# Optimization experiments

Hardware: AMD Instinct MI355X
Metric: run time of the kernel (lower is better)

Reference implementation:

```python
import jax, jax.numpy as jnp
import numpy as np

B, S, D = 1, 4096, 1024
H, DH = 8, 128
SCALING = 256.0 ** -0.5
SOFTCAP = 50.0
WINDOW = 512
EPS = 1e-6
NEG = -1e30


def setup_inputs() -> dict:
    key = jax.random.key(0)
    ks = jax.random.split(key, 8)
    hidden_states = jax.random.normal(ks[0], (B, S, D), dtype=jnp.float32)
    # rope tables: plausible cos/sin in [-1,1]
    inv_freq = 1.0 / (10000.0 ** (jnp.arange(0, DH, 2, dtype=jnp.float32) / DH))
    t = jnp.arange(S, dtype=jnp.float32)
    freqs = jnp.outer(t, inv_freq)  # [S, DH/2]
    emb = jnp.concatenate([freqs, freqs], axis=-1)  # [S, DH]
    cos = jnp.cos(emb)[None]  # [1, S, DH]
    sin = jnp.sin(emb)[None]
    w = 0.02
    Wq = jax.random.normal(ks[1], (H * DH, D), dtype=jnp.float32) * w
    Wk = jax.random.normal(ks[2], (H * DH, D), dtype=jnp.float32) * w
    Wv = jax.random.normal(ks[3], (H * DH, D), dtype=jnp.float32) * w
    Wo = jax.random.normal(ks[4], (D, H * DH), dtype=jnp.float32) * w
    q_norm_w = jnp.zeros((DH,), dtype=jnp.float32)
    k_norm_w = jnp.zeros((DH,), dtype=jnp.float32)
    return {"hidden_states": hidden_states, "cos": cos, "sin": sin,
            "Wq": Wq, "Wk": Wk, "Wv": Wv, "Wo": Wo,
            "q_norm_w": q_norm_w, "k_norm_w": k_norm_w}


def _rms_norm(x, w):
    # Gemma3 RMSNorm: x * rsqrt(mean(x^2) + eps) * (1 + w)
    var = jnp.mean(jnp.square(x), axis=-1, keepdims=True)
    return x * jax.lax.rsqrt(var + EPS) * (1.0 + w)


def _rotate_half(x):
    x1, x2 = jnp.split(x, 2, axis=-1)
    return jnp.concatenate([-x2, x1], axis=-1)


def reference(hidden_states, cos, sin, Wq, Wk, Wv, Wo, q_norm_w, k_norm_w):
    b, s, _ = hidden_states.shape
    # QKV projections -> [B, H, S, DH]
    q = (hidden_states @ Wq.T).reshape(b, s, H, DH).transpose(0, 2, 1, 3)
    k = (hidden_states @ Wk.T).reshape(b, s, H, DH).transpose(0, 2, 1, 3)
    v = (hidden_states @ Wv.T).reshape(b, s, H, DH).transpose(0, 2, 1, 3)
    # per-head RMSNorm on q and k
    q = _rms_norm(q, q_norm_w)
    k = _rms_norm(k, k_norm_w)
    # RoPE (cos/sin broadcast over heads via unsqueeze(1))
    c = cos[:, None, :, :]
    si = sin[:, None, :, :]
    q = q * c + _rotate_half(q) * si
    k = k * c + _rotate_half(k) * si
    # scores with scaling and logit softcapping
    scores = jnp.einsum('bhqd,bhkd->bhqk', q, k) * SCALING
    scores = SOFTCAP * jnp.tanh(scores / SOFTCAP)
    # causal + sliding-window mask: attend to j with 0 <= i - j < WINDOW (plus j == i)
    i = jnp.arange(s)[:, None]
    j = jnp.arange(s)[None, :]
    mask = (j <= i) & (i - j < WINDOW)  # [S, S]
    scores = jnp.where(mask[None, None], scores, NEG)
    probs = jax.nn.softmax(scores, axis=-1)  # [B, H, S, S]
    attn = jnp.einsum('bhqk,bhkd->bhqd', probs, v)
    attn = attn.transpose(0, 2, 1, 3).reshape(b, s, H * DH)
    out = attn @ Wo.T
    return out, probs
```

## Files before the change

kernel.cpp:

```cpp
#include <hip/hip_runtime.h>

#define S_LEN 4096

typedef _Float16 f16;
typedef __bf16 bf16;
typedef __attribute__((ext_vector_type(4))) _Float16 f16x4;
typedef __attribute__((ext_vector_type(8))) _Float16 f16x8;
typedef __attribute__((ext_vector_type(8))) __bf16 bf16x8;
typedef __attribute__((ext_vector_type(4))) float f32x4;

__device__ __forceinline__ void async_cp16(void* lds, const void* g) {
  __builtin_amdgcn_global_load_lds((const __attribute__((address_space(1))) void*)g,
                                   (__attribute__((address_space(3))) void*)lds, 16, 0, 0);
}

__device__ __forceinline__ f32x4 mfma16(f16x8 a, f16x8 b, f32x4 c) {
  return __builtin_amdgcn_mfma_f32_16x16x32_f16(a, b, c, 0, 0, 0);
}

__global__ void detect_dtype(const unsigned short* __restrict__ x, int* __restrict__ flag) {
  const int t = threadIdx.x;
  int cnt = 0;
  for (int i = t; i < 16384; i += 256) {
    const int e = (x[i] >> 7) & 0xFF;
    cnt += (e >= 0x87);
  }
#pragma unroll
  for (int m = 1; m < 64; m <<= 1) cnt += __shfl_xor(cnt, m);
  __shared__ int red[4];
  if ((t & 63) == 0) red[t >> 6] = cnt;
  __syncthreads();
  if (t == 0) *flag = (red[0] + red[1] + red[2] + red[3] > 64) ? 1 : 0;
}

__device__ __forceinline__ void cvt8(const void* src, f16* dst, int i, int fp) {
  f16x8 o;
  if (fp) {
    const float* s = (const float*)src;
#pragma unroll
    for (int j = 0; j < 8; ++j) o[j] = (f16)s[i + j];
  } else {
    const bf16x8 v = *(const bf16x8*)((const bf16*)src + i);
#pragma unroll
    for (int j = 0; j < 8; ++j) o[j] = (f16)(float)v[j];
  }
  *(f16x8*)(dst + i) = o;
}

__global__ void cvt_all(const void* __restrict__ hs, const void* __restrict__ wq,
                        const void* __restrict__ wk, const void* __restrict__ wv,
                        const void* __restrict__ wo, const void* __restrict__ c,
                        const void* __restrict__ s, const void* __restrict__ qn,
                        const void* __restrict__ kn, f16* __restrict__ hsf,
                        f16* __restrict__ wqkv, f16* __restrict__ woh,
                        float* __restrict__ cd, float* __restrict__ sd,
                        float* __restrict__ qnd, float* __restrict__ knd,
                        const int* __restrict__ flagp) {
  const int fp = *flagp;
  const int b = blockIdx.x, tid = threadIdx.x;
  if (b < 2048) {
    cvt8(hs, hsf, (b * 256 + tid) * 8, fp);
  } else if (b < 4096) {
    const int bb = b - 2048;
    const int sub = bb >> 9;
    const int i = ((bb & 511) * 256 + tid) * 8;
    const void* src = (sub == 0) ? wq : (sub == 1) ? wk : (sub == 2) ? wv : wo;
    f16* dst = (sub < 3) ? (wqkv + (size_t)sub * 1048576) : woh;
    cvt8(src, dst, i, fp);
  } else if (b < 8192) {
    const int bb = b - 4096;
    const void* src = (bb < 2048) ? c : s;
    float* dst = (bb < 2048) ? cd : sd;
    const int i = (bb & 2047) * 256 + tid;
    dst[i] = fp ? ((const float*)src)[i] : (float)((const bf16*)src)[i];
  } else {
    if (tid < 128) qnd[tid] = fp ? ((const float*)qn)[tid] : (float)((const bf16*)qn)[tid];
    else knd[tid - 128] = fp ? ((const float*)kn)[tid - 128] : (float)((const bf16*)kn)[tid - 128];
  }
}

__device__ __forceinline__ void probs_zero_fill(void* dout, int fp, int fb, int nfb) {
  const int tid = threadIdx.x;
  if (fp) {
    float* pb = (float*)dout + 4194304;
    const int total = 8 * 4096 * 880;
    const f32x4 z = {};
    for (int u = fb * 256 + tid; u < total; u += nfb * 256) {
      const int rowid = (int)((unsigned)u / 880u);
      const int cu = u - rowid * 880;
      const int row = rowid & 4095;
      const int q0r = row & ~63;
      const int jc0 = (q0r >= 512) ? (((q0r - 511) >> 6) << 6) : 0;
      const int jc0c = jc0 >> 2;
      const int c4 = (cu < jc0c) ? (cu << 2) : (jc0 + 576 + ((cu - jc0c) << 2));
      __builtin_nontemporal_store(z, (f32x4*)&pb[((size_t)rowid << 12) + c4]);
    }
  } else {
    bf16* pb = (bf16*)dout + 4194304;
    const int total = 8 * 4096 * 440;
    const bf16x8 z = {};
    for (int u = fb * 256 + tid; u < total; u += nfb * 256) {
      const int rowid = (int)((unsigned)u / 440u);
      const int cu = u - rowid * 440;
      const int row = rowid & 4095;
      const int q0r = row & ~63;
      const int jc0 = (q0r >= 512) ? (((q0r - 511) >> 6) << 6) : 0;
      const int jc0c = jc0 >> 3;
      const int c8 = (cu < jc0c) ? (cu << 3) : (jc0 + 576 + ((cu - jc0c) << 3));
      __builtin_nontemporal_store(z, (bf16x8*)&pb[((size_t)rowid << 12) + c8]);
    }
  }
}

__launch_bounds__(256, 2)
__global__ void gemm_qkv(const f16* __restrict__ A, const f16* __restrict__ B,
                         const float* __restrict__ cosp, const float* __restrict__ sinp,
                         const float* __restrict__ qnw, const float* __restrict__ knw,
                         f16* __restrict__ qh, f16* __restrict__ kh, f16* __restrict__ vt,
                         void* __restrict__ dout, const int* __restrict__ flagp) {
  __shared__ f16 smem[16384];
  const int id = blockIdx.x;
  if (id >= 768) {
    probs_zero_fill(dout, *flagp, id - 768, gridDim.x - 768);
    return;
  }
  f16* As = smem;
  f16* Bs = smem + 8192;
  const int tid = threadIdx.x;
  const int w = tid >> 6, l = tid & 63;
  const int n0 = (id % 24) * 128, m0 = (id / 24) * 128;
  const int wm = (w >> 1) * 64, wn = (w & 1) * 64;
  f32x4 acc[4][4] = {};
  for (int k0 = 0; k0 < 1024; k0 += 64) {
#pragma unroll
    for (int it = 0; it < 4; ++it) {
      const int c = it * 4 + w;
      const int row = c * 8 + (l >> 3);
      const int dq = (l & 7) ^ (row & 7);
      async_cp16(&As[c * 512], &A[(size_t)(m0 + row) * 1024 + k0 + dq * 8]);
      async_cp16(&Bs[c * 512], &B[(size_t)(n0 + row) * 1024 + k0 + dq * 8]);
    }
    __syncthreads();
#pragma unroll
    for (int ks = 0; ks < 2; ++ks) {
      f16x8 af[4], bfr[4];
#pragma unroll
      for (int i = 0; i < 4; ++i) {
        const int ra = wm + i * 16 + (l & 15);
        af[i] = *(const f16x8*)&As[ra * 64 + (((ks * 4 + (l >> 4)) ^ (ra & 7)) << 3)];
        const int rb = wn + i * 16 + (l & 15);
        bfr[i] = *(const f16x8*)&Bs[rb * 64 + (((ks * 4 + (l >> 4)) ^ (rb & 7)) << 3)];
      }
#pragma unroll
      for (int mi = 0; mi < 4; ++mi)
#pragma unroll
        for (int ni = 0; ni < 4; ++ni)
          acc[mi][ni] = mfma16(af[mi], bfr[ni], acc[mi][ni]);
    }
    __syncthreads();
  }
  const int part = (id % 24) >> 3;
  const int h = id & 7;
#pragma unroll
  for (int mi = 0; mi < 4; ++mi)
#pragma unroll
    for (int ni = 0; ni < 4; ++ni) {
      const int col = wn + ni * 16 + (l & 15);
#pragma unroll
      for (int r = 0; r < 4; ++r) {
        const int row = wm + mi * 16 + ((l >> 4) << 2) + r;
        smem[row * 128 + (col ^ (((row >> 3) & 7) << 3))] = (f16)acc[mi][ni][r];
      }
    }
  __syncthreads();
  if (part == 2) {
#pragma unroll
    for (int it = 0; it < 8; ++it) {
      const int idx = it * 256 + tid;
      const int dh = idx >> 4;
      const int sl = (idx & 15) * 8;
      f16x8 o;
#pragma unroll
      for (int k = 0; k < 8; ++k)
        o[k] = smem[(sl + k) * 128 + (dh ^ ((((sl + k) >> 3) & 7) << 3))];
      *(f16x8*)&vt[((size_t)(h * 128 + dh)) * S_LEN + m0 + sl] = o;
    }
  } else {
    const float* nw = part ? knw : qnw;
    f16* outb = part ? kh : qh;
    const float nw0 = 1.f + nw[l], nw1 = 1.f + nw[l + 64];
#pragma unroll 4
    for (int rr = 0; rr < 32; ++rr) {
      const int row = w * 32 + rr;
      const int sg = m0 + row;
      const int cs = ((row >> 3) & 7) << 3;
      const float x0 = (float)smem[row * 128 + (l ^ cs)];
      const float x1 = (float)smem[row * 128 + ((l + 64) ^ cs)];
      float ssum = x0 * x0 + x1 * x1;
#pragma unroll
      for (int m = 1; m < 64; m <<= 1) ssum += __shfl_xor(ssum, m);
      const float rn = rsqrtf(ssum * (1.f / 128.f) + 1e-6f);
      const float g0 = rn * nw0, g1 = rn * nw1;
      const float c0 = cosp[sg * 128 + l], c1 = cosp[sg * 128 + l + 64];
      const float s0 = sinp[sg * 128 + l], s1 = sinp[sg * 128 + l + 64];
      f16* o = outb + ((size_t)h * S_LEN + sg) * 128;
      o[l] = (f16)(x0 * g0 * c0 - x1 * g1 * s0);
      o[l + 64] = (f16)(x1 * g1 * c1 + x0 * g0 * s1);
    }
  }
}

__launch_bounds__(256, 2)
__global__ void attn64(const f16* __restrict__ Qh, const f16* __restrict__ Kh,
                       const f16* __restrict__ Vt, f16* __restrict__ Pc,
                       float* __restrict__ Lsg, f16* __restrict__ Oh) {
  __shared__ f16 Qs[64 * 128];
  __shared__ f16 Ks[2 * 64 * 128];
  __shared__ f16 Vs[2 * 128 * 64];
  const int tid = threadIdx.x, w = tid >> 6, l = tid & 63;
  const int q0 = blockIdx.x * 64, h = blockIdx.y;
  const int kt0 = (q0 >= 512) ? ((q0 - 511) >> 6) : 0;
  const int kt1 = (q0 + 64) >> 6;

#pragma unroll
  for (int it = 0; it < 4; ++it) {
    const int c = it * 4 + w;
    const int row = c * 4 + (l >> 4);
    const int dq = (l & 15) ^ (row & 15);
    async_cp16(&Qs[c * 512], &Qh[((size_t)h * S_LEN + q0 + row) * 128 + dq * 8]);
  }
#pragma unroll
  for (int it = 0; it < 4; ++it) {
    const int c = it * 4 + w;
    { const int row = c * 4 + (l >> 4);
      const int dq = (l & 15) ^ (row & 15);
      async_cp16(&Ks[c * 512], &Kh[((size_t)h * S_LEN + kt0 * 64 + row) * 128 + dq * 8]); }
    { const int row = c * 8 + (l >> 3);
      const int dq = (l & 7) ^ (row & 7);
      async_cp16(&Vs[c * 512], &Vt[((size_t)h * 128 + row) * S_LEN + kt0 * 64 + dq * 8]); }
  }
  __syncthreads();
  f16x8 qfrag[4];
#pragma unroll
  for (int ks = 0; ks < 4; ++ks) {
    const int r = w * 16 + (l & 15);
    qfrag[ks] = *(const f16x8*)&Qs[r * 128 + (((ks * 4 + (l >> 4)) ^ (r & 15)) << 3)];
  }
  __syncthreads();

  f16* Ps = Qs + w * 1024;
  float l_i[4] = {0.f, 0.f, 0.f, 0.f};
  f32x4 oacc[8] = {};

  for (int t = kt0; t < kt1; ++t) {
    const int cur = (t - kt0) & 1;
    const int kb = cur * 8192, vb = cur * 8192;
    if (t + 1 < kt1) {
      const int nb = (cur ^ 1) * 8192;
#pragma unroll
      for (int it = 0; it < 4; ++it) {
        const int c = it * 4 + w;
        { const int row = c * 4 + (l >> 4);
          const int dq = (l & 15) ^ (row & 15);
          async_cp16(&Ks[nb + c * 512],
                     &Kh[((size_t)h * S_LEN + (t + 1) * 64 + row) * 128 + dq * 8]); }
        { const int row = c * 8 + (l >> 3);
          const int dq = (l & 7) ^ (row & 7);
          async_cp16(&Vs[nb + c * 512],
                     &Vt[((size_t)h * 128 + row) * S_LEN + (t + 1) * 64 + dq * 8]); }
      }
    }
    f32x4 sacc[4] = {};
    __builtin_amdgcn_s_setprio(1);
#pragma unroll
    for (int ks = 0; ks < 4; ++ks) {
      f16x8 kfrag[4];
#pragma unroll
      for (int ni = 0; ni < 4; ++ni) {
        const int r = ni * 16 + (l & 15);
        kfrag[ni] = *(const f16x8*)&Ks[kb + r * 128 + (((ks * 4 + (l >> 4)) ^ (r & 15)) << 3)];
      }
#pragma unroll
      for (int ni = 0; ni < 4; ++ni)
        sacc[ni] = mfma16(qfrag[ks], kfrag[ni], sacc[ni]);
    }
    __builtin_amdgcn_s_setprio(0);
#pragma unroll
    for (int reg = 0; reg < 4; ++reg) {
      const int pr = ((l >> 4) << 2) + reg;
      const int q = q0 + w * 16 + pr;
      float rs = 0.f;
#pragma unroll
      for (int ni = 0; ni < 4; ++ni) {
        const int col = t * 64 + ni * 16 + (l & 15);
        float s = sacc[ni][reg] * 0.0625f;
        const float z = __expf(s * 0.04f);
        s = 50.f * (1.f - 2.f / (z + 1.f));
        const bool valid = (col <= q) && (q - col < 512);
        const float p = valid ? __expf(s - 8.f) : 0.f;
        rs += p;
        const int pc = ni * 16 + (l & 15);
        Ps[pr * 64 + (((pc >> 3) ^ (pr & 7)) << 3) + (pc & 7)] = (f16)p;
      }
#pragma unroll
      for (int m = 1; m < 16; m <<= 1) rs += __shfl_xor(rs, m);
      l_i[reg] += rs;
    }
    __builtin_amdgcn_s_setprio(1);
#pragma unroll
    for (int ks = 0; ks < 2; ++ks) {
      const int rp = l & 15;
      const f16x8 pf = *(const f16x8*)&Ps[rp * 64 + (((ks * 4 + (l >> 4)) ^ (rp & 7)) << 3)];
      f16x8 vf[8];
#pragma unroll
      for (int ni = 0; ni < 8; ++ni) {
        const int r = ni * 16 + (l & 15);
        vf[ni] = *(const f16x8*)&Vs[vb + r * 64 + (((ks * 4 + (l >> 4)) ^ (r & 7)) << 3)];
      }
#pragma unroll
      for (int ni = 0; ni < 8; ++ni)
        oacc[ni] = mfma16(pf, vf[ni], oacc[ni]);
    }
    __builtin_amdgcn_s_setprio(0);
    {
      const size_t rowbase = (size_t)h * 4096 + q0 + w * 16;
#pragma unroll
      for (int i = 0; i < 4; ++i) {
        const int pr = i * 4 + (l >> 4);
        const int pc = (l & 15) * 4;
        const f16x4 v = *(const f16x4*)&Ps[pr * 64 + (((pc >> 3) ^ (pr & 7)) << 3) + (pc & 7)];
        *(f16x4*)&Pc[(rowbase + pr) * 576 + (t - kt0) * 64 + pc] = v;
      }
    }
    __syncthreads();
  }

  float il[4];
#pragma unroll
  for (int r = 0; r < 4; ++r) il[r] = 1.f / l_i[r];
  if ((l & 15) == 0) {
#pragma unroll
    for (int r = 0; r < 4; ++r)
      Lsg[(h << 12) + q0 + w * 16 + ((l >> 4) << 2) + r] = il[r];
  }
#pragma unroll
  for (int ni = 0; ni < 8; ++ni) {
    const int row = q0 + w * 16 + ((l >> 4) << 2);
    const int col = h * 128 + ni * 16 + (l & 15);
#pragma unroll
    for (int r = 0; r < 4; ++r)
      Oh[(size_t)(row + r) * 1024 + col] = (f16)(oacc[ni][r] * il[r]);
  }
}

__launch_bounds__(256, 2)
__global__ void gemmO_probs(const f16* __restrict__ A, const f16* __restrict__ B,
                            void* __restrict__ dout, const f16* __restrict__ Pc,
                            const float* __restrict__ Lsg, const int* __restrict__ flagp) {
  __shared__ f16 smem[16384];
  const int fp = *flagp;
  const int tid = threadIdx.x;
  if (blockIdx.x < 256) {
    f16* As = smem;
    f16* Bs = smem + 8192;
    const int w = tid >> 6, l = tid & 63;
    const int n0 = (blockIdx.x & 7) * 128, m0 = (blockIdx.x >> 3) * 128;
    const int wm = (w >> 1) * 64, wn = (w & 1) * 64;
    f32x4 acc[4][4] = {};
    for (int k0 = 0; k0 < 1024; k0 += 64) {
#pragma unroll
      for (int it = 0; it < 4; ++it) {
        const int c = it * 4 + w;
        const int row = c * 8 + (l >> 3);
        const int dq = (l & 7) ^ (row & 7);
        async_cp16(&As[c * 512], &A[(size_t)(m0 + row) * 1024 + k0 + dq * 8]);
        async_cp16(&Bs[c * 512], &B[(size_t)(n0 + row) * 1024 + k0 + dq * 8]);
      }
      __syncthreads();
#pragma unroll
      for (int ks = 0; ks < 2; ++ks) {
        f16x8 af[4], bfr[4];
#pragma unroll
        for (int i = 0; i < 4; ++i) {
          const int ra = wm + i * 16 + (l & 15);
          af[i] = *(const f16x8*)&As[ra * 64 + (((ks * 4 + (l >> 4)) ^ (ra & 7)) << 3)];
          const int rb = wn + i * 16 + (l & 15);
          bfr[i] = *(const f16x8*)&Bs[rb * 64 + (((ks * 4 + (l >> 4)) ^ (rb & 7)) << 3)];
        }
#pragma unroll
        for (int mi = 0; mi < 4; ++mi)
#pragma unroll
          for (int ni = 0; ni < 4; ++ni)
            acc[mi][ni] = mfma16(af[mi], bfr[ni], acc[mi][ni]);
      }
      __syncthreads();
    }
#pragma unroll
    for (int mi = 0; mi < 4; ++mi)
#pragma unroll
      for (int ni = 0; ni < 4; ++ni) {
        const int col = n0 + wn + ni * 16 + (l & 15);
        const int row = m0 + wm + mi * 16 + ((l >> 4) << 2);
#pragma unroll
        for (int r = 0; r < 4; ++r) {
          const size_t off = (size_t)(row + r) * 1024 + col;
          if (fp) ((float*)dout)[off] = acc[mi][ni][r];
          else    ((bf16*)dout)[off] = (bf16)acc[mi][ni][r];
        }
      }
  } else {
    const int bb = blockIdx.x - 256, nbb = gridDim.x - 256;
    if (fp) {
      float* pb = (float*)dout + 4194304;
      const int total = 8 * 4096 * 144;
      for (int u = bb * 256 + tid; u < total; u += nbb * 256) {
        const int rowid = (int)((unsigned)u / 144u);
        const int cu = u - rowid * 144;
        const int row = rowid & 4095;
        const int q0r = row & ~63;
        const int jc0 = (q0r >= 512) ? (((q0r - 511) >> 6) << 6) : 0;
        const int c4 = jc0 + (cu << 2);
        f32x4 v = {};
        if (c4 < q0r + 64) {
          const float sc = Lsg[rowid];
          const f16x4 pv = *(const f16x4*)&Pc[(size_t)rowid * 576 + (cu << 2)];
#pragma unroll
          for (int k = 0; k < 4; ++k) v[k] = (float)pv[k] * sc;
        }
        __builtin_nontemporal_store(v, (f32x4*)&pb[((size_t)rowid << 12) + c4]);
      }
    } else {
      bf16* pb = (bf16*)dout + 4194304;
      const int total = 8 * 4096 * 72;
      for (int u = bb * 256 + tid; u < total; u += nbb * 256) {
        const int rowid = (int)((unsigned)u / 72u);
        const int cu = u - rowid * 72;
        const int row = rowid & 4095;
        const int q0r = row & ~63;
        const int jc0 = (q0r >= 512) ? (((q0r - 511) >> 6) << 6) : 0;
        const int c8 = jc0 + (cu << 3);
        bf16x8 v = {};
        if (c8 < q0r + 64) {
          const float sc = Lsg[rowid];
          const f16x8 pv = *(const f16x8*)&Pc[(size_t)rowid * 576 + (cu << 3)];
#pragma unroll
          for (int k = 0; k < 8; ++k) v[k] = (bf16)((float)pv[k] * sc);
        }
        __builtin_nontemporal_store(v, (bf16x8*)&pb[((size_t)rowid << 12) + c8]);
      }
    }
  }
}

extern "C" void kernel_launch(void* const* d_in, const int* in_sizes, int n_in,
                              void* d_out, int out_size, void* d_ws, size_t ws_size,
                              hipStream_t stream) {
  (void)in_sizes; (void)n_in; (void)out_size; (void)ws_size;
  char* ws = (char*)d_ws;
  f16*   Pc    = (f16*)(ws);
  f16*   qh    = (f16*)(ws + (36u << 20));
  f16*   kh    = (f16*)(ws + (44u << 20));
  f16*   vt    = (f16*)(ws + (52u << 20));
  f16*   attnh = (f16*)(ws + (60u << 20));
  f16*   woh   = (f16*)(ws + (68u << 20));
  f16*   hsf   = (f16*)(ws + (70u << 20));
  float* Lsg   = (float*)(ws + (70u << 20));
  f16*   wqkv  = (f16*)(ws + (78u << 20));
  float* cosf  = (float*)(ws + (84u << 20));
  float* sinf  = (float*)(ws + (86u << 20));
  float* qnwf  = (float*)(ws + (88u << 20));
  float* knwf  = (float*)(ws + (88u << 20) + 512);
  int*   flag  = (int*)(ws + (88u << 20) + 1024);

  detect_dtype<<<1, 256, 0, stream>>>((const unsigned short*)d_in[0], flag);
  cvt_all<<<8193, 256, 0, stream>>>(d_in[0], d_in[3], d_in[4], d_in[5], d_in[6],
                                    d_in[1], d_in[2], d_in[7], d_in[8],
                                    hsf, wqkv, woh, cosf, sinf, qnwf, knwf, flag);
  gemm_qkv<<<2048, 256, 0, stream>>>(hsf, wqkv, cosf, sinf, qnwf, knwf, qh, kh, vt,
                                     d_out, flag);
  attn64<<<dim3(64, 8), 256, 0, stream>>>(qh, kh, vt, Pc, Lsg, attnh);
  gemmO_probs<<<768, 256, 0, stream>>>(attnh, woh, d_out, Pc, Lsg, flag);
}
```

Baseline: 676.7 us.

## Move probs zero-fill into output GEMM kernel and single-buffer attention K/V

The zero-fill of the masked region of the probs output moves out of the QKV GEMM launch and into the final output-projection kernel. There it is interleaved by block index with the Wo GEMM tiles and the probs scatter, so the GEMM tiles are spread across the grid. The attention kernel drops its double-buffered K/V prefetch in favour of single-buffered loads followed by a barrier, and its occupancy hint rises from 2 to 3 blocks. The goal is to free the QKV GEMM from the store traffic, overlap the zero-fill with the compute-bound output GEMM, and raise attention occupancy. The cost is the loss of load/compute overlap inside attention.

```diff
diff --git a/kernel.cpp b/kernel.cpp
--- a/kernel.cpp
+++ b/kernel.cpp
@@ -79,56 +79,17 @@
   }
 }
 
-__device__ __forceinline__ void probs_zero_fill(void* dout, int fp, int fb, int nfb) {
-  const int tid = threadIdx.x;
-  if (fp) {
-    float* pb = (float*)dout + 4194304;
-    const int total = 8 * 4096 * 880;
-    const f32x4 z = {};
-    for (int u = fb * 256 + tid; u < total; u += nfb * 256) {
-      const int rowid = (int)((unsigned)u / 880u);
-      const int cu = u - rowid * 880;
-      const int row = rowid & 4095;
-      const int q0r = row & ~63;
-      const int jc0 = (q0r >= 512) ? (((q0r - 511) >> 6) << 6) : 0;
-      const int jc0c = jc0 >> 2;
-      const int c4 = (cu < jc0c) ? (cu << 2) : (jc0 + 576 + ((cu - jc0c) << 2));
-      __builtin_nontemporal_store(z, (f32x4*)&pb[((size_t)rowid << 12) + c4]);
-    }
-  } else {
-    bf16* pb = (bf16*)dout + 4194304;
-    const int total = 8 * 4096 * 440;
-    const bf16x8 z = {};
-    for (int u = fb * 256 + tid; u < total; u += nfb * 256) {
-      const int rowid = (int)((unsigned)u / 440u);
-      const int cu = u - rowid * 440;
-      const int row = rowid & 4095;
-      const int q0r = row & ~63;
-      const int jc0 = (q0r >= 512) ? (((q0r - 511) >> 6) << 6) : 0;
-      const int jc0c = jc0 >> 3;
-      const int c8 = (cu < jc0c) ? (cu << 3) : (jc0 + 576 + ((cu - jc0c) << 3));
-      __builtin_nontemporal_store(z, (bf16x8*)&pb[((size_t)rowid << 12) + c8]);
-    }
-  }
-}
-
 __launch_bounds__(256, 2)
 __global__ void gemm_qkv(const f16* __restrict__ A, const f16* __restrict__ B,
                          const float* __restrict__ cosp, const float* __restrict__ sinp,
                          const float* __restrict__ qnw, const float* __restrict__ knw,
-                         f16* __restrict__ qh, f16* __restrict__ kh, f16* __restrict__ vt,
-                         void* __restrict__ dout, const int* __restrict__ flagp) {
+                         f16* __restrict__ qh, f16* __restrict__ kh, f16* __restrict__ vt) {
   __shared__ f16 smem[16384];
-  const int id = blockIdx.x;
-  if (id >= 768) {
-    probs_zero_fill(dout, *flagp, id - 768, gridDim.x - 768);
-    return;
-  }
   f16* As = smem;
   f16* Bs = smem + 8192;
   const int tid = threadIdx.x;
   const int w = tid >> 6, l = tid & 63;
-  const int n0 = (id % 24) * 128, m0 = (id / 24) * 128;
+  const int n0 = blockIdx.x * 128, m0 = blockIdx.y * 128;
   const int wm = (w >> 1) * 64, wn = (w & 1) * 64;
   f32x4 acc[4][4] = {};
   for (int k0 = 0; k0 < 1024; k0 += 64) {
@@ -159,8 +120,8 @@
     }
     __syncthreads();
   }
-  const int part = (id % 24) >> 3;
-  const int h = id & 7;
+  const int part = blockIdx.x >> 3;
+  const int h = blockIdx.x & 7;
 #pragma unroll
   for (int mi = 0; mi < 4; ++mi)
 #pragma unroll
@@ -210,13 +171,13 @@
   }
 }
 
-__launch_bounds__(256, 2)
+__launch_bounds__(256, 3)
 __global__ void attn64(const f16* __restrict__ Qh, const f16* __restrict__ Kh,
                        const f16* __restrict__ Vt, f16* __restrict__ Pc,
                        float* __restrict__ Lsg, f16* __restrict__ Oh) {
   __shared__ f16 Qs[64 * 128];
-  __shared__ f16 Ks[2 * 64 * 128];
-  __shared__ f16 Vs[2 * 128 * 64];
+  __shared__ f16 Ks[64 * 128];
+  __shared__ f16 Vs[128 * 64];
   const int tid = threadIdx.x, w = tid >> 6, l = tid & 63;
   const int q0 = blockIdx.x * 64, h = blockIdx.y;
   const int kt0 = (q0 >= 512) ? ((q0 - 511) >> 6) : 0;
@@ -229,16 +190,6 @@
     const int dq = (l & 15) ^ (row & 15);
     async_cp16(&Qs[c * 512], &Qh[((size_t)h * S_LEN + q0 + row) * 128 + dq * 8]);
   }
-#pragma unroll
-  for (int it = 0; it < 4; ++it) {
-    const int c = it * 4 + w;
-    { const int row = c * 4 + (l >> 4);
-      const int dq = (l & 15) ^ (row & 15);
-      async_cp16(&Ks[c * 512], &Kh[((size_t)h * S_LEN + kt0 * 64 + row) * 128 + dq * 8]); }
-    { const int row = c * 8 + (l >> 3);
-      const int dq = (l & 7) ^ (row & 7);
-      async_cp16(&Vs[c * 512], &Vt[((size_t)h * 128 + row) * S_LEN + kt0 * 64 + dq * 8]); }
-  }
   __syncthreads();
   f16x8 qfrag[4];
 #pragma unroll
@@ -253,23 +204,17 @@
   f32x4 oacc[8] = {};
 
   for (int t = kt0; t < kt1; ++t) {
-    const int cur = (t - kt0) & 1;
-    const int kb = cur * 8192, vb = cur * 8192;
-    if (t + 1 < kt1) {
-      const int nb = (cur ^ 1) * 8192;
-#pragma unroll
-      for (int it = 0; it < 4; ++it) {
-        const int c = it * 4 + w;
-        { const int row = c * 4 + (l >> 4);
-          const int dq = (l & 15) ^ (row & 15);
-          async_cp16(&Ks[nb + c * 512],
-                     &Kh[((size_t)h * S_LEN + (t + 1) * 64 + row) * 128 + dq * 8]); }
-        { const int row = c * 8 + (l >> 3);
-          const int dq = (l & 7) ^ (row & 7);
-          async_cp16(&Vs[nb + c * 512],
-                     &Vt[((size_t)h * 128 + row) * S_LEN + (t + 1) * 64 + dq * 8]); }
-      }
-    }
+#pragma unroll
+    for (int it = 0; it < 4; ++it) {
+      const int c = it * 4 + w;
+      { const int row = c * 4 + (l >> 4);
+        const int dq = (l & 15) ^ (row & 15);
+        async_cp16(&Ks[c * 512], &Kh[((size_t)h * S_LEN + t * 64 + row) * 128 + dq * 8]); }
+      { const int row = c * 8 + (l >> 3);
+        const int dq = (l & 7) ^ (row & 7);
+        async_cp16(&Vs[c * 512], &Vt[((size_t)h * 128 + row) * S_LEN + t * 64 + dq * 8]); }
+    }
+    __syncthreads();
     f32x4 sacc[4] = {};
     __builtin_amdgcn_s_setprio(1);
 #pragma unroll
@@ -278,7 +223,7 @@
 #pragma unroll
       for (int ni = 0; ni < 4; ++ni) {
         const int r = ni * 16 + (l & 15);
-        kfrag[ni] = *(const f16x8*)&Ks[kb + r * 128 + (((ks * 4 + (l >> 4)) ^ (r & 15)) << 3)];
+        kfrag[ni] = *(const f16x8*)&Ks[r * 128 + (((ks * 4 + (l >> 4)) ^ (r & 15)) << 3)];
       }
 #pragma unroll
       for (int ni = 0; ni < 4; ++ni)
@@ -315,7 +260,7 @@
 #pragma unroll
       for (int ni = 0; ni < 8; ++ni) {
         const int r = ni * 16 + (l & 15);
-        vf[ni] = *(const f16x8*)&Vs[vb + r * 64 + (((ks * 4 + (l >> 4)) ^ (r & 7)) << 3)];
+        vf[ni] = *(const f16x8*)&Vs[r * 64 + (((ks * 4 + (l >> 4)) ^ (r & 7)) << 3)];
       }
 #pragma unroll
       for (int ni = 0; ni < 8; ++ni)
@@ -360,11 +305,14 @@
   __shared__ f16 smem[16384];
   const int fp = *flagp;
   const int tid = threadIdx.x;
-  if (blockIdx.x < 256) {
+  const int id = blockIdx.x;
+  const int r8 = id & 7;
+  if (r8 == 0) {
+    const int bid = id >> 3;
     f16* As = smem;
     f16* Bs = smem + 8192;
     const int w = tid >> 6, l = tid & 63;
-    const int n0 = (blockIdx.x & 7) * 128, m0 = (blockIdx.x >> 3) * 128;
+    const int n0 = (bid & 7) * 128, m0 = (bid >> 3) * 128;
     const int wm = (w >> 1) * 64, wn = (w & 1) * 64;
     f32x4 acc[4][4] = {};
     for (int k0 = 0; k0 < 1024; k0 += 64) {
@@ -408,12 +356,12 @@
           else    ((bf16*)dout)[off] = (bf16)acc[mi][ni][r];
         }
       }
-  } else {
-    const int bb = blockIdx.x - 256, nbb = gridDim.x - 256;
+  } else if (r8 <= 2) {
+    const int fb = (id >> 3) * 2 + (r8 - 1), nfb = 512;
     if (fp) {
       float* pb = (float*)dout + 4194304;
       const int total = 8 * 4096 * 144;
-      for (int u = bb * 256 + tid; u < total; u += nbb * 256) {
+      for (int u = fb * 256 + tid; u < total; u += nfb * 256) {
         const int rowid = (int)((unsigned)u / 144u);
         const int cu = u - rowid * 144;
         const int row = rowid & 4095;
@@ -432,7 +380,7 @@
     } else {
       bf16* pb = (bf16*)dout + 4194304;
       const int total = 8 * 4096 * 72;
-      for (int u = bb * 256 + tid; u < total; u += nbb * 256) {
+      for (int u = fb * 256 + tid; u < total; u += nfb * 256) {
         const int rowid = (int)((unsigned)u / 72u);
         const int cu = u - rowid * 72;
         const int row = rowid & 4095;
@@ -447,6 +395,37 @@
           for (int k = 0; k < 8; ++k) v[k] = (bf16)((float)pv[k] * sc);
         }
         __builtin_nontemporal_store(v, (bf16x8*)&pb[((size_t)rowid << 12) + c8]);
+      }
+    }
+  } else {
+    const int fb = (id >> 3) * 5 + (r8 - 3), nfb = 1280;
+    if (fp) {
+      float* pb = (float*)dout + 4194304;
+      const int total = 8 * 4096 * 880;
+      const f32x4 z = {};
+      for (int u = fb * 256 + tid; u < total; u += nfb * 256) {
+        const int rowid = (int)((unsigned)u / 880u);
+        const int cu = u - rowid * 880;
+        const int row = rowid & 4095;
+        const int q0r = row & ~63;
+        const int jc0 = (q0r >= 512) ? (((q0r - 511) >> 6) << 6) : 0;
+        const int jc0c = jc0 >> 2;
+        const int c4 = (cu < jc0c) ? (cu << 2) : (jc0 + 576 + ((cu - jc0c) << 2));
+        __builtin_nontemporal_store(z, (f32x4*)&pb[((size_t)rowid << 12) + c4]);
+      }
+    } else {
+      bf16* pb = (bf16*)dout + 4194304;
+      const int total = 8 * 4096 * 440;
+      const bf16x8 z = {};
+      for (int u = fb * 256 + tid; u < total; u += nfb * 256) {
+        const int rowid = (int)((unsigned)u / 440u);
+        const int cu = u - rowid * 440;
+        const int row = rowid & 4095;
+        const int q0r = row & ~63;
+        const int jc0 = (q0r >= 512) ? (((q0r - 511) >> 6) << 6) : 0;
+        const int jc0c = jc0 >> 3;
+        const int c8 = (cu < jc0c) ? (cu << 3) : (jc0 + 576 + ((cu - jc0c) << 3));
+        __builtin_nontemporal_store(z, (bf16x8*)&pb[((size_t)rowid << 12) + c8]);
       }
     }
   }
@@ -476,8 +455,7 @@
   cvt_all<<<8193, 256, 0, stream>>>(d_in[0], d_in[3], d_in[4], d_in[5], d_in[6],
                                     d_in[1], d_in[2], d_in[7], d_in[8],
                                     hsf, wqkv, woh, cosf, sinf, qnwf, knwf, flag);
-  gemm_qkv<<<2048, 256, 0, stream>>>(hsf, wqkv, cosf, sinf, qnwf, knwf, qh, kh, vt,
-                                     d_out, flag);
+  gemm_qkv<<<dim3(24, 32), 256, 0, stream>>>(hsf, wqkv, cosf, sinf, qnwf, knwf, qh, kh, vt);
   attn64<<<dim3(64, 8), 256, 0, stream>>>(qh, kh, vt, Pc, Lsg, attnh);
-  gemmO_probs<<<768, 256, 0, stream>>>(attnh, woh, d_out, Pc, Lsg, flag);
-}
+  gemmO_probs<<<2048, 256, 0, stream>>>(attnh, woh, d_out, Pc, Lsg, flag);
+}
```

Result: no change. 674.5 us (-0.3%).
